# Kernel tuning notes

Hardware: AMD Instinct MI355X
Metric: run time of the kernel (lower is better)

The kernel has to match this reference:

```python
import jax, jax.numpy as jnp
import numpy as np

N_NODES = 100000
N_EDGES = 200000
IN_FEATS = 1024
H_FEATS = 512
N_HEADS = 4
HEAD_DIM = H_FEATS // N_HEADS  # 128
N_CLASSES = 2983
BATCH = 1024


def setup_inputs() -> dict:
    key = jax.random.key(0)
    ks = jax.random.split(key, 24)
    x = jax.random.normal(ks[0], (N_NODES, IN_FEATS), jnp.float32)
    e1_src = jax.random.randint(ks[1], (N_EDGES,), 0, N_NODES)
    e1_dst = jax.random.randint(ks[2], (N_EDGES,), 0, N_NODES)
    e2_src = jax.random.randint(ks[3], (N_EDGES,), 0, N_NODES)
    e2_dst = jax.random.randint(ks[4], (N_EDGES,), 0, N_NODES)

    def lin_w(k, fin, fout):
        return jax.random.normal(k, (fin, fout), jnp.float32) * np.float32(1.0 / np.sqrt(fin))

    def att_w(k):
        return jax.random.normal(k, (N_HEADS, HEAD_DIM), jnp.float32) * np.float32(0.1)

    inp = dict(x=x, e1_src=e1_src, e1_dst=e1_dst, e2_src=e2_src, e2_dst=e2_dst,
               batch_size=BATCH)
    # layer 0 (in_feats -> h_feats), one GATConv per edge type
    inp["w0a"] = lin_w(ks[5], IN_FEATS, H_FEATS); inp["as0a"] = att_w(ks[6]); inp["ad0a"] = att_w(ks[7]); inp["b0a"] = jnp.zeros((H_FEATS,), jnp.float32)
    inp["w0b"] = lin_w(ks[8], IN_FEATS, H_FEATS); inp["as0b"] = att_w(ks[9]); inp["ad0b"] = att_w(ks[10]); inp["b0b"] = jnp.zeros((H_FEATS,), jnp.float32)
    # layer 1 (h_feats -> h_feats)
    inp["w1a"] = lin_w(ks[11], H_FEATS, H_FEATS); inp["as1a"] = att_w(ks[12]); inp["ad1a"] = att_w(ks[13]); inp["b1a"] = jnp.zeros((H_FEATS,), jnp.float32)
    inp["w1b"] = lin_w(ks[14], H_FEATS, H_FEATS); inp["as1b"] = att_w(ks[15]); inp["ad1b"] = att_w(ks[16]); inp["b1b"] = jnp.zeros((H_FEATS,), jnp.float32)
    # classification head
    inp["lin_w"] = lin_w(ks[17], H_FEATS, N_CLASSES)
    inp["lin_b"] = jnp.zeros((N_CLASSES,), jnp.float32)
    return inp


def gat_conv(x, src, dst, W, a_src, a_dst, b):
    """PyG GATConv (add_self_loops=False, concat=True, attn negative_slope=0.2)."""
    h = (x @ W).reshape(-1, N_HEADS, HEAD_DIM)          # [N, H, C]
    alpha_src = jnp.einsum('nhc,hc->nh', h, a_src)       # [N, H]
    alpha_dst = jnp.einsum('nhc,hc->nh', h, a_dst)       # [N, H]
    e = jax.nn.leaky_relu(alpha_src[src] + alpha_dst[dst], 0.2)   # [E, H]
    # segment softmax over incoming edges of each destination node
    m = jax.ops.segment_max(e, dst, num_segments=N_NODES)          # [N, H]
    ex = jnp.exp(e - m[dst])
    denom = jax.ops.segment_sum(ex, dst, num_segments=N_NODES)     # [N, H]
    alpha = ex / denom[dst]                                        # [E, H]
    msg = alpha[:, :, None] * h[src]                               # [E, H, C]
    out = jax.ops.segment_sum(msg, dst, num_segments=N_NODES)      # [N, H, C]
    return out.reshape(-1, N_HEADS * HEAD_DIM) + b


def reference(x, e1_src, e1_dst, e2_src, e2_dst, batch_size,
              w0a, as0a, ad0a, b0a, w0b, as0b, ad0b, b0b,
              w1a, as1a, ad1a, b1a, w1b, as1b, ad1b, b1b,
              lin_w, lin_b):
    # layer 0: HeteroConv sums per-edge-type GATConv outputs on 'paper'
    h1 = gat_conv(x, e1_src, e1_dst, w0a, as0a, ad0a, b0a) \
       + gat_conv(x, e2_src, e2_dst, w0b, as0b, ad0b, b0b)
    h1 = jax.nn.leaky_relu(h1, 0.01)   # F.leaky_relu default slope; dropout is identity in eval
    # layer 1
    h2 = gat_conv(h1, e1_src, e1_dst, w1a, as1a, ad1a, b1a) \
       + gat_conv(h1, e2_src, e2_dst, w1b, as1b, ad1b, b1b)
    # classification head on the seed nodes
    return h2[:batch_size] @ lin_w + lin_b
```

## Files before the change

kernel.cpp:

```cpp
#include <hip/hip_runtime.h>

#define N_NODES 100000
#define N_EDGES 200000
#define IN_FEATS 1024
#define H_FEATS 512
#define N_HEADS 4
#define HEAD_DIM 128
#define N_CLASSES 2983
#define BATCH 1024

typedef __attribute__((ext_vector_type(8))) short short8;
typedef __attribute__((ext_vector_type(4))) float floatx4;

typedef __attribute__((address_space(1))) void global_as_void;
typedef __attribute__((address_space(3))) void lds_as_void;

__device__ __forceinline__ float bf2f(unsigned short u) {
    union { unsigned int i; float f; } x; x.i = ((unsigned int)u) << 16; return x.f;
}
__device__ __forceinline__ unsigned short f2bf(float f) {
    union { float f; unsigned int i; } x; x.f = f;
    unsigned int r = x.i + 0x7FFFu + ((x.i >> 16) & 1u);
    return (unsigned short)(r >> 16);
}
__device__ __forceinline__ void load_lds16(const void* g, void* l) {
    __builtin_amdgcn_global_load_lds((const global_as_void*)g, (lds_as_void*)l, 16, 0, 0);
}

__global__ __launch_bounds__(256, 3)
void gemm_kernel(const void* __restrict__ Ain, int a_fp32, int a_dense,
                 const unsigned short* __restrict__ BT,
                 void* __restrict__ Cout, const float* __restrict__ bias,
                 const float* __restrict__ att_s, const float* __restrict__ att_d,
                 const float* __restrict__ att_s2, const float* __restrict__ att_d2,
                 float* __restrict__ asrc, float* __restrict__ adst,
                 const int* __restrict__ rowlist, const int* __restrict__ countp,
                 int M, int N, int n_tiles, int K, int out_bf16)
{
    __shared__ __attribute__((aligned(16))) unsigned short As[128 * 32];
    __shared__ __attribute__((aligned(16))) unsigned short Bs[128 * 32];
    __shared__ float attbuf[128][4];
    const int tid  = threadIdx.x;
    const int lane = tid & 63;
    const int wave = tid >> 6;
    const int bid = blockIdx.x;
    int mt, nt;
    if (n_tiles == 8) {
        mt = (bid & 7) + ((bid >> 6) << 3);
        nt = (bid >> 3) & 7;
    } else {
        mt = bid / n_tiles;
        nt = bid - mt * n_tiles;
    }
    const int m0 = mt * 128;
    const int n0 = nt * 128;
    int Mv = M;
    if (countp) Mv = countp[0];
    if (m0 >= Mv) return;
    const int wr = (wave >> 1) * 64;
    const int wc = (wave & 1) * 64;
    const int lm = lane & 15;
    const int quad = lane >> 4;

    auto arow = [&](int r) -> int {
        int gr = m0 + r; if (gr > Mv - 1) gr = Mv - 1;
        if (rowlist && !a_dense) gr = rowlist[gr];
        return gr;
    };

    const float* a_fp[2];
    const unsigned short* a_bf[2];
    char* a_lds[2];
    const unsigned short* b_bf[2];
    char* b_lds[2];
    if (a_fp32) {
        int row = tid >> 2, slot = tid & 3;
#pragma unroll
        for (int p = 0; p < 2; p++) {
            int r = p * 64 + row;
            a_fp[p] = (const float*)Ain + (size_t)arow(r) * K + (slot ^ ((r >> 1) & 3)) * 8;
        }
    } else {
#pragma unroll
        for (int i = 0; i < 2; i++) {
            int r = wave * 32 + i * 16 + (lane >> 2);
            a_bf[i] = (const unsigned short*)Ain + (size_t)arow(r) * K
                    + ((lane & 3) ^ ((r >> 1) & 3)) * 8;
            a_lds[i] = (char*)As + (size_t)(wave * 2 + i) * 1024;
        }
    }
#pragma unroll
    for (int i = 0; i < 2; i++) {
        int r = wave * 32 + i * 16 + (lane >> 2);
        int gn = n0 + r; if (gn > N - 1) gn = N - 1;
        b_bf[i] = BT + (size_t)gn * K + ((lane & 3) ^ ((r >> 1) & 3)) * 8;
        b_lds[i] = (char*)Bs + (size_t)(wave * 2 + i) * 1024;
    }

    floatx4 acc[4][4];
#pragma unroll
    for (int i = 0; i < 4; i++)
#pragma unroll
        for (int j = 0; j < 4; j++) acc[i][j] = (floatx4)0.0f;

    for (int k0 = 0; k0 < K; k0 += 32) {
        __syncthreads();
        if (a_fp32) {
            int row = tid >> 2, slot = tid & 3;
#pragma unroll
            for (int p = 0; p < 2; p++) {
                int r = p * 64 + row;
                floatx4 f0 = *(const floatx4*)(a_fp[p] + k0);
                floatx4 f1 = *(const floatx4*)(a_fp[p] + k0 + 4);
                short8 v;
                v[0] = (short)f2bf(f0[0]); v[1] = (short)f2bf(f0[1]);
                v[2] = (short)f2bf(f0[2]); v[3] = (short)f2bf(f0[3]);
                v[4] = (short)f2bf(f1[0]); v[5] = (short)f2bf(f1[1]);
                v[6] = (short)f2bf(f1[2]); v[7] = (short)f2bf(f1[3]);
                *(short8*)&As[r * 32 + slot * 8] = v;
            }
        } else {
#pragma unroll
            for (int i = 0; i < 2; i++)
                load_lds16(a_bf[i] + k0, a_lds[i]);
        }
#pragma unroll
        for (int i = 0; i < 2; i++)
            load_lds16(b_bf[i] + k0, b_lds[i]);
        __syncthreads();
        short8 af[4], bfr[4];
#pragma unroll
        for (int i = 0; i < 4; i++) {
            int ra = wr + i * 16 + lm;
            af[i] = *(const short8*)&As[ra * 32 + ((quad ^ ((ra >> 1) & 3)) << 3)];
            int rb = wc + i * 16 + lm;
            bfr[i] = *(const short8*)&Bs[rb * 32 + ((quad ^ ((rb >> 1) & 3)) << 3)];
        }
#pragma unroll
        for (int i = 0; i < 4; i++)
#pragma unroll
            for (int j = 0; j < 4; j++)
                acc[i][j] = __builtin_amdgcn_mfma_f32_16x16x32_bf16(af[i], bfr[j], acc[i][j], 0, 0, 0);
    }

    if (att_s) {
        const int h = nt;
        const float* wsp = (h < 4) ? att_s : att_s2;
        const float* wdp = (h < 4) ? att_d : att_d2;
        const int hh = h & 3;
        const int half2 = (wc >> 6) * 2;
#pragma unroll
        for (int i = 0; i < 4; i++) {
#pragma unroll
            for (int r = 0; r < 4; r++) {
                float ss = 0.f, sd = 0.f;
#pragma unroll
                for (int j = 0; j < 4; j++) {
                    int c = wc + j * 16 + lm;
                    ss += acc[i][j][r] * wsp[hh * HEAD_DIM + c];
                    sd += acc[i][j][r] * wdp[hh * HEAD_DIM + c];
                }
#pragma unroll
                for (int off = 1; off < 16; off <<= 1) {
                    ss += __shfl_xor(ss, off);
                    sd += __shfl_xor(sd, off);
                }
                if (lm == 0) {
                    int rl = wr + i * 16 + quad * 4 + r;
                    attbuf[rl][half2]     = ss;
                    attbuf[rl][half2 + 1] = sd;
                }
            }
        }
        __syncthreads();
        if (tid < 128) {
            int grl = m0 + tid;
            if (grl < Mv) {
                int gr = rowlist ? rowlist[grl] : grl;
                asrc[(size_t)gr * 8 + h] = attbuf[tid][0] + attbuf[tid][2];
                adst[(size_t)gr * 8 + h] = attbuf[tid][1] + attbuf[tid][3];
            }
        }
    }

#pragma unroll
    for (int i = 0; i < 4; i++) {
        int grb = wr + i * 16 + quad * 4;
#pragma unroll
        for (int j = 0; j < 4; j++) {
            int gc = n0 + wc + j * 16 + lm;
            if (gc < N) {
#pragma unroll
                for (int r = 0; r < 4; r++) {
                    int grl = m0 + grb + r;
                    if (grl < Mv) {
                        int gr = rowlist ? rowlist[grl] : grl;
                        float v = acc[i][j][r];
                        if (out_bf16) {
                            ((unsigned short*)Cout)[(size_t)gr * N + gc] = f2bf(v);
                        } else {
                            float b = bias ? bias[gc] : 0.0f;
                            ((float*)Cout)[(size_t)gr * N + gc] = v + b;
                        }
                    }
                }
            }
        }
    }
}

__global__ void cvt_rows_kernel(const float* __restrict__ X, const int* __restrict__ list,
                                const int* __restrict__ countp, unsigned short* __restrict__ Y)
{
    int n0 = countp[0];
    int col = (threadIdx.x & 127) * 8;
    for (int i = blockIdx.x * 2 + (threadIdx.x >> 7); i < n0; i += gridDim.x * 2) {
        const floatx4* xp = (const floatx4*)(X + (size_t)list[i] * IN_FEATS + col);
        floatx4 f0 = xp[0], f1 = xp[1];
        short8 v;
        v[0] = (short)f2bf(f0[0]); v[1] = (short)f2bf(f0[1]);
        v[2] = (short)f2bf(f0[2]); v[3] = (short)f2bf(f0[3]);
        v[4] = (short)f2bf(f1[0]); v[5] = (short)f2bf(f1[1]);
        v[6] = (short)f2bf(f1[2]); v[7] = (short)f2bf(f1[3]);
        *(short8*)(Y + (size_t)i * IN_FEATS + col) = v;
    }
}

__global__ void hist2_kernel(const int* __restrict__ e1d, const int* __restrict__ e2d,
                             int* __restrict__ cnt2, int E)
{
    int e = blockIdx.x * blockDim.x + threadIdx.x;
    if (e < E) {
        atomicAdd(&cnt2[e1d[e]], 1);
        atomicAdd(&cnt2[N_NODES + e2d[e]], 1);
    }
}

__global__ void scan1_kernel(const int* __restrict__ cnt, int* __restrict__ partial,
                             int* __restrict__ chunksum, int n)
{
    __shared__ int sm[256];
    int t = threadIdx.x;
    int i = blockIdx.x * 256 + t;
    int v = (i < n) ? cnt[i] : 0;
    sm[t] = v; __syncthreads();
    int val = v;
#pragma unroll
    for (int off = 1; off < 256; off <<= 1) {
        int u = (t >= off) ? sm[t - off] : 0;
        __syncthreads();
        val += u; sm[t] = val;
        __syncthreads();
    }
    if (i < n) partial[i] = val - v;
    if (t == 255) chunksum[blockIdx.x] = val;
}

__global__ void scan2_kernel(int* __restrict__ chunksum, int n)
{
    __shared__ int sm[1024];
    int t = threadIdx.x;
    int v = (t < n) ? chunksum[t] : 0;
    sm[t] = v; __syncthreads();
    int val = v;
#pragma unroll
    for (int off = 1; off < 1024; off <<= 1) {
        int u = (t >= off) ? sm[t - off] : 0;
        __syncthreads();
        val += u; sm[t] = val;
        __syncthreads();
    }
    if (t < n) chunksum[t] = val - v;
}

__global__ void scan3c_kernel(const int* __restrict__ partial, const int* __restrict__ chunksum,
                              int* __restrict__ rowptrc, int* __restrict__ cursor, int n, int Etot)
{
    int i = blockIdx.x * 256 + threadIdx.x;
    if (i < n) {
        int r = partial[i] + chunksum[i >> 8];
        rowptrc[i] = r;
        cursor[i] = r;
    }
    if (i == 0) rowptrc[n] = Etot;
}

__global__ void fill2_kernel(const int* __restrict__ e1s, const int* __restrict__ e1d,
                             const int* __restrict__ e2s, const int* __restrict__ e2d,
                             int* __restrict__ cursor, int* __restrict__ srcsc, int E)
{
    int e = blockIdx.x * blockDim.x + threadIdx.x;
    if (e < E) {
        int p = atomicAdd(&cursor[e1d[e]], 1);
        srcsc[p] = e1s[e];
        int q = atomicAdd(&cursor[N_NODES + e2d[e]], 1);
        srcsc[q] = e2s[e];
    }
}

__global__ void mark1_kernel(const int* __restrict__ e1s, const int* __restrict__ e1d,
                             const int* __restrict__ e2s, const int* __restrict__ e2d,
                             int* __restrict__ flag1, int E)
{
    int e = blockIdx.x * blockDim.x + threadIdx.x;
    if (e >= E) return;
    if (e < BATCH) flag1[e] = 1;
    if (e1d[e] < BATCH) flag1[e1s[e]] = 1;
    if (e2d[e] < BATCH) flag1[e2s[e]] = 1;
}

__global__ void mark0_kernel(const int* __restrict__ e1s, const int* __restrict__ e1d,
                             const int* __restrict__ e2s, const int* __restrict__ e2d,
                             const int* __restrict__ flag1, int* __restrict__ flag0,
                             int E, int Nn)
{
    int i = blockIdx.x * blockDim.x + threadIdx.x;
    if (i < E) {
        if (flag1[e1d[i]]) flag0[e1s[i]] = 1;
        if (flag1[e2d[i]]) flag0[e2s[i]] = 1;
    }
    if (i < Nn && flag1[i]) flag0[i] = 1;
}

__global__ void compactF_kernel(const int* __restrict__ flag, const int* __restrict__ partial,
                                const int* __restrict__ chunksum,
                                int* __restrict__ list1, int* __restrict__ list0,
                                int* __restrict__ count1, int* __restrict__ count0)
{
    int i = blockIdx.x * 256 + threadIdx.x;
    if (i >= 2 * N_NODES) return;
    int total1 = partial[N_NODES] + chunksum[N_NODES >> 8];
    int pos = partial[i] + chunksum[i >> 8];
    if (i < N_NODES) {
        if (flag[i]) list1[pos] = i;
        if (i == 0) count1[0] = total1;
    } else {
        if (flag[i]) list0[pos - total1] = i - N_NODES;
        if (i == 2 * N_NODES - 1) count0[0] = pos + flag[i] - total1;
    }
}

__global__ void gather2_kernel(const int* __restrict__ rowptrc, const int* __restrict__ srcsc,
                               const float* __restrict__ asrc, const float* __restrict__ adst,
                               const unsigned short* __restrict__ H,
                               const float* __restrict__ b1, const float* __restrict__ b2,
                               const int* __restrict__ dlist, const int* __restrict__ dcountp,
                               unsigned short* __restrict__ Out, int ndst, int do_lrelu)
{
    int nd = dcountp ? dcountp[0] : ndst;
    int lane = threadIdx.x & 63;
    int head = lane >> 4;
    int col = lane * 8;
    for (int i = blockIdx.x * 4 + (threadIdx.x >> 6); i < nd; i += gridDim.x * 4) {
        int d = dlist ? dlist[i] : i;
        float r[8], acc[8];
        {
            int beg = rowptrc[d], end = rowptrc[d + 1];
            float ad = adst[(size_t)d * 8 + head];
            float den = 0.f;
#pragma unroll
            for (int k = 0; k < 8; k++) acc[k] = 0.f;
            for (int j = beg; j < end; j++) {
                int s = srcsc[j];
                float v = asrc[(size_t)s * 8 + head] + ad;
                v = v > 0.f ? v : 0.2f * v;
                float ex = expf(v);
                den += ex;
                short8 hv = *(const short8*)(H + (size_t)s * 1024 + col);
#pragma unroll
                for (int k = 0; k < 8; k++) acc[k] += ex * bf2f((unsigned short)hv[k]);
            }
            float inv = den > 0.f ? 1.f / den : 0.f;
#pragma unroll
            for (int k = 0; k < 8; k++) r[k] = acc[k] * inv;
        }
        {
            int beg = rowptrc[N_NODES + d], end = rowptrc[N_NODES + d + 1];
            float ad = adst[(size_t)d * 8 + 4 + head];
            float den = 0.f;
#pragma unroll
            for (int k = 0; k < 8; k++) acc[k] = 0.f;
            for (int j = beg; j < end; j++) {
                int s = srcsc[j];
                float v = asrc[(size_t)s * 8 + 4 + head] + ad;
                v = v > 0.f ? v : 0.2f * v;
                float ex = expf(v);
                den += ex;
                short8 hv = *(const short8*)(H + (size_t)s * 1024 + 512 + col);
#pragma unroll
                for (int k = 0; k < 8; k++) acc[k] += ex * bf2f((unsigned short)hv[k]);
            }
            float inv = den > 0.f ? 1.f / den : 0.f;
#pragma unroll
            for (int k = 0; k < 8; k++) r[k] += acc[k] * inv;
        }
        short8 o;
#pragma unroll
        for (int k = 0; k < 8; k++) {
            float f = r[k] + b1[col + k] + b2[col + k];
            if (do_lrelu) f = f > 0.f ? f : 0.01f * f;
            o[k] = (short)f2bf(f);
        }
        *(short8*)(Out + (size_t)i * 512 + col) = o;
    }
}

__global__ void transpose2_kernel(const float* __restrict__ Wa, const float* __restrict__ Wb,
                                  unsigned short* __restrict__ WT, int K, int Nh)
{
    int k = blockIdx.x * 256 + threadIdx.x;
    if (k >= K) return;
    int n = blockIdx.y;
    const float* W = (n < Nh) ? Wa : Wb;
    int nn = (n < Nh) ? n : n - Nh;
    WT[(size_t)n * K + k] = f2bf(W[(size_t)k * Nh + nn]);
}

extern "C" void kernel_launch(void* const* d_in, const int* in_sizes, int n_in,
                              void* d_out, int out_size, void* d_ws, size_t ws_size,
                              hipStream_t stream)
{
    const float* x    = (const float*)d_in[0];
    const int* e1s    = (const int*)d_in[1];
    const int* e1d    = (const int*)d_in[2];
    const int* e2s    = (const int*)d_in[3];
    const int* e2d    = (const int*)d_in[4];
    const float* w0a  = (const float*)d_in[6];
    const float* as0a = (const float*)d_in[7];
    const float* ad0a = (const float*)d_in[8];
    const float* b0a  = (const float*)d_in[9];
    const float* w0b  = (const float*)d_in[10];
    const float* as0b = (const float*)d_in[11];
    const float* ad0b = (const float*)d_in[12];
    const float* b0b  = (const float*)d_in[13];
    const float* w1a  = (const float*)d_in[14];
    const float* as1a = (const float*)d_in[15];
    const float* ad1a = (const float*)d_in[16];
    const float* b1a  = (const float*)d_in[17];
    const float* w1b  = (const float*)d_in[18];
    const float* as1b = (const float*)d_in[19];
    const float* ad1b = (const float*)d_in[20];
    const float* b1b  = (const float*)d_in[21];
    const float* linw = (const float*)d_in[22];
    const float* linb = (const float*)d_in[23];
    float* out = (float*)d_out;
    (void)in_sizes; (void)n_in; (void)out_size;

    char* ws = (char*)d_ws;
    size_t off = 0;
    auto carve = [&](size_t bytes) -> void* {
        void* p = ws + off; off += (bytes + 255) & ~(size_t)255; return p;
    };
    unsigned short* WT0 = (unsigned short*)carve((size_t)2 * H_FEATS * IN_FEATS * 2);
    unsigned short* WT1 = (unsigned short*)carve((size_t)2 * H_FEATS * H_FEATS * 2);
    unsigned short* WTl = (unsigned short*)carve((size_t)N_CLASSES * H_FEATS * 2);
    unsigned short* Hbf = (unsigned short*)carve((size_t)N_NODES * 1024 * 2);
    unsigned short* H1c = (unsigned short*)carve((size_t)N_NODES * H_FEATS * 2);
    unsigned short* h2s = (unsigned short*)carve((size_t)BATCH * H_FEATS * 2);
    float* asrc = (float*)carve((size_t)N_NODES * 8 * 4);
    float* adst = (float*)carve((size_t)N_NODES * 8 * 4);
    int* rowptrc = (int*)carve((size_t)(2 * N_NODES + 1) * 4);
    int* srcsc   = (int*)carve((size_t)2 * N_EDGES * 4);
    int* cnt2    = (int*)carve((size_t)2 * N_NODES * 4);
    int* partial = (int*)carve((size_t)2 * N_NODES * 4);
    int* chunksum= (int*)carve((size_t)1024 * 4);
    int* flagbuf = (int*)carve((size_t)2 * N_NODES * 4);
    int* list1   = (int*)carve((size_t)N_NODES * 4);
    int* list0   = (int*)carve((size_t)N_NODES * 4);
    int* count1  = (int*)carve(256);
    int* count0  = (int*)carve(256);
    unsigned short* xc = nullptr;
    {
        size_t need = (size_t)N_NODES * IN_FEATS * 2;
        if (off + need <= ws_size) xc = (unsigned short*)carve(need);
    }

    const int NCHUNK2 = (2 * N_NODES + 255) / 256;
    const int MT8 = (((N_NODES + 127) / 128) + 7) & ~7;
    const int EG = (N_EDGES + 255) / 256;

    transpose2_kernel<<<dim3(IN_FEATS / 256, 2 * H_FEATS), 256, 0, stream>>>(w0a, w0b, WT0, IN_FEATS, H_FEATS);
    transpose2_kernel<<<dim3(H_FEATS / 256, 2 * H_FEATS), 256, 0, stream>>>(w1a, w1b, WT1, H_FEATS, H_FEATS);
    transpose2_kernel<<<dim3(H_FEATS / 256, N_CLASSES), 256, 0, stream>>>(linw, linw, WTl, H_FEATS, N_CLASSES);

    hipMemsetAsync(flagbuf, 0, (size_t)2 * N_NODES * 4, stream);
    mark1_kernel<<<EG, 256, 0, stream>>>(e1s, e1d, e2s, e2d, flagbuf, N_EDGES);
    mark0_kernel<<<EG, 256, 0, stream>>>(e1s, e1d, e2s, e2d, flagbuf, flagbuf + N_NODES,
                                         N_EDGES, N_NODES);
    scan1_kernel<<<NCHUNK2, 256, 0, stream>>>(flagbuf, partial, chunksum, 2 * N_NODES);
    scan2_kernel<<<1, 1024, 0, stream>>>(chunksum, NCHUNK2);
    compactF_kernel<<<NCHUNK2, 256, 0, stream>>>(flagbuf, partial, chunksum,
                                                 list1, list0, count1, count0);

    hipMemsetAsync(cnt2, 0, (size_t)2 * N_NODES * 4, stream);
    hist2_kernel<<<EG, 256, 0, stream>>>(e1d, e2d, cnt2, N_EDGES);
    scan1_kernel<<<NCHUNK2, 256, 0, stream>>>(cnt2, partial, chunksum, 2 * N_NODES);
    scan2_kernel<<<1, 1024, 0, stream>>>(chunksum, NCHUNK2);
    scan3c_kernel<<<NCHUNK2, 256, 0, stream>>>(partial, chunksum, rowptrc, cnt2,
                                               2 * N_NODES, 2 * N_EDGES);
    fill2_kernel<<<EG, 256, 0, stream>>>(e1s, e1d, e2s, e2d, cnt2, srcsc, N_EDGES);

    if (xc) {
        cvt_rows_kernel<<<1024, 256, 0, stream>>>(x, list0, count0, xc);
    }

    if (xc) {
        gemm_kernel<<<MT8 * 8, 256, 0, stream>>>(xc, 0, 1, WT0, Hbf, nullptr,
                                                 as0a, ad0a, as0b, ad0b, asrc, adst,
                                                 list0, count0,
                                                 N_NODES, 1024, 8, IN_FEATS, 1);
    } else {
        gemm_kernel<<<MT8 * 8, 256, 0, stream>>>(x, 1, 0, WT0, Hbf, nullptr,
                                                 as0a, ad0a, as0b, ad0b, asrc, adst,
                                                 list0, count0,
                                                 N_NODES, 1024, 8, IN_FEATS, 1);
    }
    gather2_kernel<<<2048, 256, 0, stream>>>(rowptrc, srcsc, asrc, adst, Hbf, b0a, b0b,
                                             list1, count1, H1c, N_NODES, 1);

    gemm_kernel<<<MT8 * 8, 256, 0, stream>>>(H1c, 0, 1, WT1, Hbf, nullptr,
                                             as1a, ad1a, as1b, ad1b, asrc, adst,
                                             list1, count1,
                                             N_NODES, 1024, 8, H_FEATS, 1);
    gather2_kernel<<<256, 256, 0, stream>>>(rowptrc, srcsc, asrc, adst, Hbf, b1a, b1b,
                                            nullptr, nullptr, h2s, BATCH, 0);

    const int HN_T = (N_CLASSES + 127) / 128;
    gemm_kernel<<<(BATCH / 128) * HN_T, 256, 0, stream>>>(h2s, 0, 0, WTl, out, linb,
                                                          nullptr, nullptr, nullptr, nullptr,
                                                          nullptr, nullptr, nullptr, nullptr,
                                                          BATCH, N_CLASSES, HN_T, H_FEATS, 0);
}
```

Baseline: 775.8 us.

## Fuse graph preprocessing and weight transposes into fewer kernel launches

Merges the three weight-transpose kernels, the seed-marking pass and the in-degree histogram into one grid-stride prep kernel. The two independent prefix scans (flags and degree counts) now run together in shared scan kernels, and compaction is merged with row-pointer finalisation. CSR fill is merged with the bf16 row conversion. The aim is to cut kernel launches and inter-kernel gaps in the setup phase. The fused grid-stride loops may lose some parallelism, and the conversion loop now always writes, into Hbf when no spare workspace exists.

```diff
diff --git a/kernel.cpp b/kernel.cpp
--- a/kernel.cpp
+++ b/kernel.cpp
@@ -8,6 +8,7 @@
 #define HEAD_DIM 128
 #define N_CLASSES 2983
 #define BATCH 1024
+#define NCHUNK2 782
 
 typedef __attribute__((ext_vector_type(8))) short short8;
 typedef __attribute__((ext_vector_type(4))) float floatx4;
@@ -209,13 +210,144 @@
     }
 }
 
-__global__ void cvt_rows_kernel(const float* __restrict__ X, const int* __restrict__ list,
-                                const int* __restrict__ countp, unsigned short* __restrict__ Y)
-{
-    int n0 = countp[0];
+__global__ void prep1_kernel(const float* __restrict__ w0a, const float* __restrict__ w0b,
+                             const float* __restrict__ w1a, const float* __restrict__ w1b,
+                             const float* __restrict__ linw,
+                             unsigned short* __restrict__ WT0, unsigned short* __restrict__ WT1,
+                             unsigned short* __restrict__ WTl,
+                             const int* __restrict__ e1s, const int* __restrict__ e1d,
+                             const int* __restrict__ e2s, const int* __restrict__ e2d,
+                             int* __restrict__ flag1, int* __restrict__ cnt2)
+{
+    const int gsz = gridDim.x * 256;
+    const int gid = blockIdx.x * 256 + threadIdx.x;
+    for (int i = gid; i < 1024 * 1024; i += gsz) {
+        int n = i >> 10, k = i & 1023;
+        const float* W = (n < 512) ? w0a : w0b;
+        WT0[i] = f2bf(W[(size_t)k * 512 + (n & 511)]);
+    }
+    for (int i = gid; i < 1024 * 512; i += gsz) {
+        int n = i >> 9, k = i & 511;
+        const float* W = (n < 512) ? w1a : w1b;
+        WT1[i] = f2bf(W[(size_t)k * 512 + (n & 511)]);
+    }
+    for (int i = gid; i < N_CLASSES * 512; i += gsz) {
+        int n = i >> 9, k = i & 511;
+        WTl[i] = f2bf(linw[(size_t)k * N_CLASSES + n]);
+    }
+    for (int e = gid; e < N_EDGES; e += gsz) {
+        if (e < BATCH) flag1[e] = 1;
+        int d1 = e1d[e], d2 = e2d[e];
+        if (d1 < BATCH) flag1[e1s[e]] = 1;
+        if (d2 < BATCH) flag1[e2s[e]] = 1;
+        atomicAdd(&cnt2[d1], 1);
+        atomicAdd(&cnt2[N_NODES + d2], 1);
+    }
+}
+
+__global__ void mark0_kernel(const int* __restrict__ e1s, const int* __restrict__ e1d,
+                             const int* __restrict__ e2s, const int* __restrict__ e2d,
+                             const int* __restrict__ flag1, int* __restrict__ flag0,
+                             int E, int Nn)
+{
+    int i = blockIdx.x * blockDim.x + threadIdx.x;
+    if (i < E) {
+        if (flag1[e1d[i]]) flag0[e1s[i]] = 1;
+        if (flag1[e2d[i]]) flag0[e2s[i]] = 1;
+    }
+    if (i < Nn && flag1[i]) flag0[i] = 1;
+}
+
+__global__ void scanA_kernel(const int* __restrict__ flagbuf, const int* __restrict__ cnt2,
+                             int* __restrict__ partialF, int* __restrict__ chunkF,
+                             int* __restrict__ partialC, int* __restrict__ chunkC)
+{
+    __shared__ int sm[256];
+    int b = blockIdx.x;
+    const int* src; int* pdst; int* cdst; int cb;
+    if (b < NCHUNK2) { src = flagbuf; pdst = partialF; cdst = chunkF; cb = b; }
+    else             { src = cnt2;    pdst = partialC; cdst = chunkC; cb = b - NCHUNK2; }
+    int t = threadIdx.x;
+    int i = cb * 256 + t;
+    int v = (i < 2 * N_NODES) ? src[i] : 0;
+    sm[t] = v; __syncthreads();
+    int val = v;
+#pragma unroll
+    for (int off = 1; off < 256; off <<= 1) {
+        int u = (t >= off) ? sm[t - off] : 0;
+        __syncthreads();
+        val += u; sm[t] = val;
+        __syncthreads();
+    }
+    if (i < 2 * N_NODES) pdst[i] = val - v;
+    if (t == 255) cdst[cb] = val;
+}
+
+__global__ void scanB_kernel(int* __restrict__ chunkF, int* __restrict__ chunkC, int n)
+{
+    __shared__ int sm[1024];
+    int t = threadIdx.x;
+#pragma unroll
+    for (int pass = 0; pass < 2; pass++) {
+        int* c = pass ? chunkC : chunkF;
+        int v = (t < n) ? c[t] : 0;
+        sm[t] = v; __syncthreads();
+        int val = v;
+#pragma unroll
+        for (int off = 1; off < 1024; off <<= 1) {
+            int u = (t >= off) ? sm[t - off] : 0;
+            __syncthreads();
+            val += u; sm[t] = val;
+            __syncthreads();
+        }
+        if (t < n) c[t] = val - v;
+        __syncthreads();
+    }
+}
+
+__global__ void finalize_kernel(const int* __restrict__ flagbuf,
+                                const int* __restrict__ partialF, const int* __restrict__ chunkF,
+                                const int* __restrict__ partialC, const int* __restrict__ chunkC,
+                                int* __restrict__ list1, int* __restrict__ list0,
+                                int* __restrict__ count1, int* __restrict__ count0,
+                                int* __restrict__ rowptrc, int* __restrict__ cursor)
+{
+    int i = blockIdx.x * 256 + threadIdx.x;
+    if (i >= 2 * N_NODES) return;
+    int r = partialC[i] + chunkC[i >> 8];
+    rowptrc[i] = r;
+    cursor[i] = r;
+    if (i == 0) rowptrc[2 * N_NODES] = 2 * N_EDGES;
+    int total1 = partialF[N_NODES] + chunkF[N_NODES >> 8];
+    int pos = partialF[i] + chunkF[i >> 8];
+    int f = flagbuf[i];
+    if (i < N_NODES) {
+        if (f) list1[pos] = i;
+        if (i == 0) count1[0] = total1;
+    } else {
+        if (f) list0[pos - total1] = i - N_NODES;
+        if (i == 2 * N_NODES - 1) count0[0] = pos + f - total1;
+    }
+}
+
+__global__ void fill_cvt_kernel(const int* __restrict__ e1s, const int* __restrict__ e1d,
+                                const int* __restrict__ e2s, const int* __restrict__ e2d,
+                                int* __restrict__ cursor, int* __restrict__ srcsc,
+                                const float* __restrict__ X, const int* __restrict__ list0,
+                                const int* __restrict__ count0, unsigned short* __restrict__ Y)
+{
+    const int gsz = gridDim.x * 256;
+    const int gid = blockIdx.x * 256 + threadIdx.x;
+    for (int e = gid; e < N_EDGES; e += gsz) {
+        int p = atomicAdd(&cursor[e1d[e]], 1);
+        srcsc[p] = e1s[e];
+        int q = atomicAdd(&cursor[N_NODES + e2d[e]], 1);
+        srcsc[q] = e2s[e];
+    }
+    int n0 = count0[0];
     int col = (threadIdx.x & 127) * 8;
     for (int i = blockIdx.x * 2 + (threadIdx.x >> 7); i < n0; i += gridDim.x * 2) {
-        const floatx4* xp = (const floatx4*)(X + (size_t)list[i] * IN_FEATS + col);
+        const floatx4* xp = (const floatx4*)(X + (size_t)list0[i] * IN_FEATS + col);
         floatx4 f0 = xp[0], f1 = xp[1];
         short8 v;
         v[0] = (short)f2bf(f0[0]); v[1] = (short)f2bf(f0[1]);
@@ -223,120 +355,6 @@
         v[4] = (short)f2bf(f1[0]); v[5] = (short)f2bf(f1[1]);
         v[6] = (short)f2bf(f1[2]); v[7] = (short)f2bf(f1[3]);
         *(short8*)(Y + (size_t)i * IN_FEATS + col) = v;
-    }
-}
-
-__global__ void hist2_kernel(const int* __restrict__ e1d, const int* __restrict__ e2d,
-                             int* __restrict__ cnt2, int E)
-{
-    int e = blockIdx.x * blockDim.x + threadIdx.x;
-    if (e < E) {
-        atomicAdd(&cnt2[e1d[e]], 1);
-        atomicAdd(&cnt2[N_NODES + e2d[e]], 1);
-    }
-}
-
-__global__ void scan1_kernel(const int* __restrict__ cnt, int* __restrict__ partial,
-                             int* __restrict__ chunksum, int n)
-{
-    __shared__ int sm[256];
-    int t = threadIdx.x;
-    int i = blockIdx.x * 256 + t;
-    int v = (i < n) ? cnt[i] : 0;
-    sm[t] = v; __syncthreads();
-    int val = v;
-#pragma unroll
-    for (int off = 1; off < 256; off <<= 1) {
-        int u = (t >= off) ? sm[t - off] : 0;
-        __syncthreads();
-        val += u; sm[t] = val;
-        __syncthreads();
-    }
-    if (i < n) partial[i] = val - v;
-    if (t == 255) chunksum[blockIdx.x] = val;
-}
-
-__global__ void scan2_kernel(int* __restrict__ chunksum, int n)
-{
-    __shared__ int sm[1024];
-    int t = threadIdx.x;
-    int v = (t < n) ? chunksum[t] : 0;
-    sm[t] = v; __syncthreads();
-    int val = v;
-#pragma unroll
-    for (int off = 1; off < 1024; off <<= 1) {
-        int u = (t >= off) ? sm[t - off] : 0;
-        __syncthreads();
-        val += u; sm[t] = val;
-        __syncthreads();
-    }
-    if (t < n) chunksum[t] = val - v;
-}
-
-__global__ void scan3c_kernel(const int* __restrict__ partial, const int* __restrict__ chunksum,
-                              int* __restrict__ rowptrc, int* __restrict__ cursor, int n, int Etot)
-{
-    int i = blockIdx.x * 256 + threadIdx.x;
-    if (i < n) {
-        int r = partial[i] + chunksum[i >> 8];
-        rowptrc[i] = r;
-        cursor[i] = r;
-    }
-    if (i == 0) rowptrc[n] = Etot;
-}
-
-__global__ void fill2_kernel(const int* __restrict__ e1s, const int* __restrict__ e1d,
-                             const int* __restrict__ e2s, const int* __restrict__ e2d,
-                             int* __restrict__ cursor, int* __restrict__ srcsc, int E)
-{
-    int e = blockIdx.x * blockDim.x + threadIdx.x;
-    if (e < E) {
-        int p = atomicAdd(&cursor[e1d[e]], 1);
-        srcsc[p] = e1s[e];
-        int q = atomicAdd(&cursor[N_NODES + e2d[e]], 1);
-        srcsc[q] = e2s[e];
-    }
-}
-
-__global__ void mark1_kernel(const int* __restrict__ e1s, const int* __restrict__ e1d,
-                             const int* __restrict__ e2s, const int* __restrict__ e2d,
-                             int* __restrict__ flag1, int E)
-{
-    int e = blockIdx.x * blockDim.x + threadIdx.x;
-    if (e >= E) return;
-    if (e < BATCH) flag1[e] = 1;
-    if (e1d[e] < BATCH) flag1[e1s[e]] = 1;
-    if (e2d[e] < BATCH) flag1[e2s[e]] = 1;
-}
-
-__global__ void mark0_kernel(const int* __restrict__ e1s, const int* __restrict__ e1d,
-                             const int* __restrict__ e2s, const int* __restrict__ e2d,
-                             const int* __restrict__ flag1, int* __restrict__ flag0,
-                             int E, int Nn)
-{
-    int i = blockIdx.x * blockDim.x + threadIdx.x;
-    if (i < E) {
-        if (flag1[e1d[i]]) flag0[e1s[i]] = 1;
-        if (flag1[e2d[i]]) flag0[e2s[i]] = 1;
-    }
-    if (i < Nn && flag1[i]) flag0[i] = 1;
-}
-
-__global__ void compactF_kernel(const int* __restrict__ flag, const int* __restrict__ partial,
-                                const int* __restrict__ chunksum,
-                                int* __restrict__ list1, int* __restrict__ list0,
-                                int* __restrict__ count1, int* __restrict__ count0)
-{
-    int i = blockIdx.x * 256 + threadIdx.x;
-    if (i >= 2 * N_NODES) return;
-    int total1 = partial[N_NODES] + chunksum[N_NODES >> 8];
-    int pos = partial[i] + chunksum[i >> 8];
-    if (i < N_NODES) {
-        if (flag[i]) list1[pos] = i;
-        if (i == 0) count1[0] = total1;
-    } else {
-        if (flag[i]) list0[pos - total1] = i - N_NODES;
-        if (i == 2 * N_NODES - 1) count0[0] = pos + flag[i] - total1;
     }
 }
 
@@ -403,17 +421,6 @@
         }
         *(short8*)(Out + (size_t)i * 512 + col) = o;
     }
-}
-
-__global__ void transpose2_kernel(const float* __restrict__ Wa, const float* __restrict__ Wb,
-                                  unsigned short* __restrict__ WT, int K, int Nh)
-{
-    int k = blockIdx.x * 256 + threadIdx.x;
-    if (k >= K) return;
-    int n = blockIdx.y;
-    const float* W = (n < Nh) ? Wa : Wb;
-    int nn = (n < Nh) ? n : n - Nh;
-    WT[(size_t)n * K + k] = f2bf(W[(size_t)k * Nh + nn]);
 }
 
 extern "C" void kernel_launch(void* const* d_in, const int* in_sizes, int n_in,
@@ -459,12 +466,14 @@
     unsigned short* h2s = (unsigned short*)carve((size_t)BATCH * H_FEATS * 2);
     float* asrc = (float*)carve((size_t)N_NODES * 8 * 4);
     float* adst = (float*)carve((size_t)N_NODES * 8 * 4);
+    int* cnt2    = (int*)carve((size_t)2 * N_NODES * 4);
+    int* flagbuf = (int*)carve((size_t)2 * N_NODES * 4);
     int* rowptrc = (int*)carve((size_t)(2 * N_NODES + 1) * 4);
     int* srcsc   = (int*)carve((size_t)2 * N_EDGES * 4);
-    int* cnt2    = (int*)carve((size_t)2 * N_NODES * 4);
-    int* partial = (int*)carve((size_t)2 * N_NODES * 4);
-    int* chunksum= (int*)carve((size_t)1024 * 4);
-    int* flagbuf = (int*)carve((size_t)2 * N_NODES * 4);
+    int* partialF= (int*)carve((size_t)2 * N_NODES * 4);
+    int* partialC= (int*)carve((size_t)2 * N_NODES * 4);
+    int* chunkF  = (int*)carve((size_t)1024 * 4);
+    int* chunkC  = (int*)carve((size_t)1024 * 4);
     int* list1   = (int*)carve((size_t)N_NODES * 4);
     int* list0   = (int*)carve((size_t)N_NODES * 4);
     int* count1  = (int*)carve(256);
@@ -475,34 +484,20 @@
         if (off + need <= ws_size) xc = (unsigned short*)carve(need);
     }
 
-    const int NCHUNK2 = (2 * N_NODES + 255) / 256;
     const int MT8 = (((N_NODES + 127) / 128) + 7) & ~7;
     const int EG = (N_EDGES + 255) / 256;
 
-    transpose2_kernel<<<dim3(IN_FEATS / 256, 2 * H_FEATS), 256, 0, stream>>>(w0a, w0b, WT0, IN_FEATS, H_FEATS);
-    transpose2_kernel<<<dim3(H_FEATS / 256, 2 * H_FEATS), 256, 0, stream>>>(w1a, w1b, WT1, H_FEATS, H_FEATS);
-    transpose2_kernel<<<dim3(H_FEATS / 256, N_CLASSES), 256, 0, stream>>>(linw, linw, WTl, H_FEATS, N_CLASSES);
-
-    hipMemsetAsync(flagbuf, 0, (size_t)2 * N_NODES * 4, stream);
-    mark1_kernel<<<EG, 256, 0, stream>>>(e1s, e1d, e2s, e2d, flagbuf, N_EDGES);
+    hipMemsetAsync(cnt2, 0, (size_t)4 * N_NODES * 4, stream);
+    prep1_kernel<<<2048, 256, 0, stream>>>(w0a, w0b, w1a, w1b, linw, WT0, WT1, WTl,
+                                           e1s, e1d, e2s, e2d, flagbuf, cnt2);
     mark0_kernel<<<EG, 256, 0, stream>>>(e1s, e1d, e2s, e2d, flagbuf, flagbuf + N_NODES,
                                          N_EDGES, N_NODES);
-    scan1_kernel<<<NCHUNK2, 256, 0, stream>>>(flagbuf, partial, chunksum, 2 * N_NODES);
-    scan2_kernel<<<1, 1024, 0, stream>>>(chunksum, NCHUNK2);
-    compactF_kernel<<<NCHUNK2, 256, 0, stream>>>(flagbuf, partial, chunksum,
-                                                 list1, list0, count1, count0);
-
-    hipMemsetAsync(cnt2, 0, (size_t)2 * N_NODES * 4, stream);
-    hist2_kernel<<<EG, 256, 0, stream>>>(e1d, e2d, cnt2, N_EDGES);
-    scan1_kernel<<<NCHUNK2, 256, 0, stream>>>(cnt2, partial, chunksum, 2 * N_NODES);
-    scan2_kernel<<<1, 1024, 0, stream>>>(chunksum, NCHUNK2);
-    scan3c_kernel<<<NCHUNK2, 256, 0, stream>>>(partial, chunksum, rowptrc, cnt2,
-                                               2 * N_NODES, 2 * N_EDGES);
-    fill2_kernel<<<EG, 256, 0, stream>>>(e1s, e1d, e2s, e2d, cnt2, srcsc, N_EDGES);
-
-    if (xc) {
-        cvt_rows_kernel<<<1024, 256, 0, stream>>>(x, list0, count0, xc);
-    }
+    scanA_kernel<<<2 * NCHUNK2, 256, 0, stream>>>(flagbuf, cnt2, partialF, chunkF, partialC, chunkC);
+    scanB_kernel<<<1, 1024, 0, stream>>>(chunkF, chunkC, NCHUNK2);
+    finalize_kernel<<<NCHUNK2, 256, 0, stream>>>(flagbuf, partialF, chunkF, partialC, chunkC,
+                                                 list1, list0, count1, count0, rowptrc, cnt2);
+    fill_cvt_kernel<<<1024, 256, 0, stream>>>(e1s, e1d, e2s, e2d, cnt2, srcsc,
+                                              x, list0, count0, xc ? xc : (unsigned short*)Hbf);
 
     if (xc) {
         gemm_kernel<<<MT8 * 8, 256, 0, stream>>>(xc, 0, 1, WT0, Hbf, nullptr,
@@ -517,14 +512,12 @@
     }
     gather2_kernel<<<2048, 256, 0, stream>>>(rowptrc, srcsc, asrc, adst, Hbf, b0a, b0b,
                                              list1, count1, H1c, N_NODES, 1);
-
     gemm_kernel<<<MT8 * 8, 256, 0, stream>>>(H1c, 0, 1, WT1, Hbf, nullptr,
                                              as1a, ad1a, as1b, ad1b, asrc, adst,
                                              list1, count1,
                                              N_NODES, 1024, 8, H_FEATS, 1);
     gather2_kernel<<<256, 256, 0, stream>>>(rowptrc, srcsc, asrc, adst, Hbf, b1a, b1b,
                                             nullptr, nullptr, h2s, BATCH, 0);
-
     const int HN_T = (N_CLASSES + 127) / 128;
     gemm_kernel<<<(BATCH / 128) * HN_T, 256, 0, stream>>>(h2s, 0, 0, WTl, out, linb,
                                                           nullptr, nullptr, nullptr, nullptr,
```

Measured after the change: 749.0 us. 3.5% less time.
